# Kernel tuning notes

Hardware: AMD Instinct MI355X
Metric: run time of the kernel (lower is better)

The kernel has to match this reference:

```python
import jax, jax.numpy as jnp
import numpy as np

N = 28  # Optics_simulation(28): fixed optical field size


def _pad_kernel_centered(w, n):
    """Zero-pad a [..., k, k] kernel to [..., n, n] centered, then ifftshift so
    that frequency-domain multiplication gives a centered ('same') circular
    convolution, matching the FFT-based 4f optical conv simulation."""
    k = w.shape[-1]
    pad = n - k
    pb = pad // 2
    pa = pad - pb
    cfg = [(0, 0)] * (w.ndim - 2) + [(pb, pa), (pb, pa)]
    wp = jnp.pad(w, cfg)
    return jnp.fft.ifftshift(wp, axes=(-2, -1))


def setup_inputs() -> dict:
    key = jax.random.key(0)
    k1, k2 = jax.random.split(key)
    B, Cin, Cout, K = 256, 256, 256, 3
    x = jax.random.normal(k1, (B, Cin, N, N), dtype=jnp.float32)
    # kaiming_uniform-ish init scale for a [Cout, Cin, K, K] kernel
    bound = 1.0 / np.sqrt(Cin * K * K)
    kernel = jax.random.uniform(k2, (Cout, Cin, K, K), dtype=jnp.float32,
                                minval=-bound, maxval=bound)
    return {"x": x, "kernel": kernel}


def reference(x, kernel):
    # Faithful to the original forward, including its indexing bug: the inner
    # loop always uses input_channel = 0, so every input channel is convolved
    # with kernel[oc, 0]. By linearity of convolution:
    #   out[b, oc] = sum_ic conv(x[b, ic], kernel[oc, 0])
    #             = conv(sum_ic x[b, ic], kernel[oc, 0])
    xs = x.sum(axis=1)                      # [B, N, N]
    w0 = kernel[:, 0]                       # [O, K, K]
    Fw = jnp.fft.fft2(_pad_kernel_centered(w0, N))   # [O, N, N] complex
    Fx = jnp.fft.fft2(xs)                            # [B, N, N] complex
    out = jnp.fft.ifft2(Fx[:, None, :, :] * Fw[None, :, :, :]).real  # [B,O,N,N]
    return out.astype(x.dtype)
```

## Files before the change

### kernel.cpp

```cpp
#include <hip/hip_runtime.h>

#define NDIM 28
#define SPAT 784
#define STRIPS 196
#define NB 256
#define CIN 256
#define COUT 256
#define SCH 4
#define CPC (CIN / SCH)
#define XSC 36

typedef float f4v __attribute__((ext_vector_type(4)));

__global__ __launch_bounds__(256) void k_sum(const float* __restrict__ x,
                                             float* __restrict__ pbuf) {
    int bid = blockIdx.x;
    int b     = bid >> 2;
    int chunk = bid & 3;
    int t = threadIdx.x;
    if (t >= STRIPS) return;

    const float4* xp = (const float4*)x
        + ((size_t)b * CIN + (size_t)chunk * CPC) * STRIPS + t;
    float ax = 0.f, ay = 0.f, az = 0.f, aw = 0.f;
    #pragma unroll 16
    for (int c = 0; c < CPC; ++c) {
        float4 v = xp[c * STRIPS];
        ax += v.x; ay += v.y; az += v.z; aw += v.w;
    }
    ((float4*)pbuf)[((size_t)b * SCH + chunk) * STRIPS + t] = make_float4(ax, ay, az, aw);
}

__global__ __launch_bounds__(256) void k_conv(const float* __restrict__ pbuf,
                                              const float* __restrict__ w,
                                              float* __restrict__ out) {
    __shared__ float xs[30 * XSC];

    int bid = blockIdx.x;
    int b  = bid >> 2;
    int cg = bid & 3;
    int t  = threadIdx.x;

    if (t < STRIPS) {
        const float4* pp = (const float4*)pbuf + (size_t)b * SCH * STRIPS + t;
        float4 a = pp[0];
        #pragma unroll
        for (int c = 1; c < SCH; ++c) {
            float4 v = pp[c * STRIPS];
            a.x += v.x; a.y += v.y; a.z += v.z; a.w += v.w;
        }
        int i = t / 7, q = t % 7;
        *(float4*)&xs[i * XSC + q * 4] = a;
        if (q == 0)
            *(float4*)&xs[i * XSC + 28] = a;
        if (i < 2) {
            *(float4*)&xs[(i + 28) * XSC + q * 4] = a;
            if (q == 0)
                *(float4*)&xs[(i + 28) * XSC + 28] = a;
        }
    }
    __syncthreads();

    if (t >= STRIPS) return;
    int i  = t / 7;
    int js = (t % 7) * 4;

    float W[3][8];
    #pragma unroll
    for (int a = 0; a < 3; ++a) {
        float4 lo = *(const float4*)&xs[(i + a) * XSC + js];
        float4 hi = *(const float4*)&xs[(i + a) * XSC + js + 4];
        W[a][0] = lo.x; W[a][1] = lo.y; W[a][2] = lo.z; W[a][3] = lo.w;
        W[a][4] = hi.x; W[a][5] = hi.y; W[a][6] = hi.z; W[a][7] = hi.w;
    }

    size_t ob = ((size_t)b * COUT + (size_t)cg * 64) * SPAT + i * NDIM + js;

    #pragma unroll 4
    for (int cl = 0; cl < 64; ++cl) {
        const float* wp = w + (size_t)(cg * 64 + cl) * (CIN * 9);
        float o0 = 0.f, o1 = 0.f, o2 = 0.f, o3 = 0.f;
        #pragma unroll
        for (int a = 0; a < 3; ++a) {
            #pragma unroll
            for (int c = 0; c < 3; ++c) {
                float fv = wp[8 - 3 * a - c];
                o0 += fv * W[a][0 + c];
                o1 += fv * W[a][1 + c];
                o2 += fv * W[a][2 + c];
                o3 += fv * W[a][3 + c];
            }
        }
        f4v o = {o0, o1, o2, o3};
        __builtin_nontemporal_store(o, (f4v*)(out + ob + (size_t)cl * SPAT));
    }
}

extern "C" void kernel_launch(void* const* d_in, const int* in_sizes, int n_in,
                              void* d_out, int out_size, void* d_ws, size_t ws_size,
                              hipStream_t stream) {
    const float* x = (const float*)d_in[0];
    const float* w = (const float*)d_in[1];
    float* out = (float*)d_out;
    float* pbuf = (float*)d_ws;

    k_sum<<<NB * SCH, 256, 0, stream>>>(x, pbuf);
    k_conv<<<NB * SCH, 256, 0, stream>>>(pbuf, w, out);
}
```

Baseline: 77.31 us.

## Pipeline channel-sum and conv over batch quarters with mixed kernels

Splits the batch into four quarters and launches kernels that run the conv for quarter q alongside the channel-sum for quarter q+1 in the same grid. This overlaps the read-heavy summation of x with the write-heavy output stores instead of running the two phases back to back. The cost is five launches instead of two, plus more per-launch overhead and tail effects.

```diff
diff --git a/kernel.cpp b/kernel.cpp
--- a/kernel.cpp
+++ b/kernel.cpp
@@ -9,17 +9,14 @@
 #define SCH 4
 #define CPC (CIN / SCH)
 #define XSC 36
+#define QB 64
 
 typedef float f4v __attribute__((ext_vector_type(4)));
 
-__global__ __launch_bounds__(256) void k_sum(const float* __restrict__ x,
-                                             float* __restrict__ pbuf) {
-    int bid = blockIdx.x;
-    int b     = bid >> 2;
-    int chunk = bid & 3;
-    int t = threadIdx.x;
+__device__ __forceinline__ void dev_sum(const float* __restrict__ x,
+                                        float* __restrict__ pbuf,
+                                        int b, int chunk, int t) {
     if (t >= STRIPS) return;
-
     const float4* xp = (const float4*)x
         + ((size_t)b * CIN + (size_t)chunk * CPC) * STRIPS + t;
     float ax = 0.f, ay = 0.f, az = 0.f, aw = 0.f;
@@ -31,16 +28,10 @@
     ((float4*)pbuf)[((size_t)b * SCH + chunk) * STRIPS + t] = make_float4(ax, ay, az, aw);
 }
 
-__global__ __launch_bounds__(256) void k_conv(const float* __restrict__ pbuf,
-                                              const float* __restrict__ w,
-                                              float* __restrict__ out) {
-    __shared__ float xs[30 * XSC];
-
-    int bid = blockIdx.x;
-    int b  = bid >> 2;
-    int cg = bid & 3;
-    int t  = threadIdx.x;
-
+__device__ __forceinline__ void dev_conv(const float* __restrict__ pbuf,
+                                         const float* __restrict__ w,
+                                         float* __restrict__ out,
+                                         float* xs, int b, int cg, int t) {
     if (t < STRIPS) {
         const float4* pp = (const float4*)pbuf + (size_t)b * SCH * STRIPS + t;
         float4 a = pp[0];
@@ -96,6 +87,33 @@
     }
 }
 
+__global__ __launch_bounds__(256) void k_sumq(const float* __restrict__ x,
+                                              float* __restrict__ pbuf, int b0) {
+    dev_sum(x, pbuf, b0 + (blockIdx.x >> 2), blockIdx.x & 3, threadIdx.x);
+}
+
+__global__ __launch_bounds__(256) void k_convq(const float* __restrict__ pbuf,
+                                               const float* __restrict__ w,
+                                               float* __restrict__ out, int b0) {
+    __shared__ float xs[30 * XSC];
+    dev_conv(pbuf, w, out, xs, b0 + (blockIdx.x >> 2), blockIdx.x & 3, threadIdx.x);
+}
+
+__global__ __launch_bounds__(256) void k_mix(const float* __restrict__ x,
+                                             float* __restrict__ pbuf,
+                                             const float* __restrict__ w,
+                                             float* __restrict__ out,
+                                             int bs0, int bc0) {
+    __shared__ float xs[30 * XSC];
+    int bid = blockIdx.x;
+    if (bid < 256) {
+        dev_conv(pbuf, w, out, xs, bc0 + (bid >> 2), bid & 3, threadIdx.x);
+    } else {
+        bid -= 256;
+        dev_sum(x, pbuf, bs0 + (bid >> 2), bid & 3, threadIdx.x);
+    }
+}
+
 extern "C" void kernel_launch(void* const* d_in, const int* in_sizes, int n_in,
                               void* d_out, int out_size, void* d_ws, size_t ws_size,
                               hipStream_t stream) {
@@ -104,6 +122,9 @@
     float* out = (float*)d_out;
     float* pbuf = (float*)d_ws;
 
-    k_sum<<<NB * SCH, 256, 0, stream>>>(x, pbuf);
-    k_conv<<<NB * SCH, 256, 0, stream>>>(pbuf, w, out);
+    k_sumq <<<256, 256, 0, stream>>>(x, pbuf, 0);
+    k_mix  <<<512, 256, 0, stream>>>(x, pbuf, w, out, 1 * QB, 0 * QB);
+    k_mix  <<<512, 256, 0, stream>>>(x, pbuf, w, out, 2 * QB, 1 * QB);
+    k_mix  <<<512, 256, 0, stream>>>(x, pbuf, w, out, 3 * QB, 2 * QB);
+    k_convq<<<256, 256, 0, stream>>>(pbuf, w, out, 3 * QB);
 }
```

Measured after the change: 74.35 us (median of 2 runs). -3.8%, faster.
